# Kernel optimization log

Measured on AMD Instinct MI355X. Metric: run time of the kernel, lower is better.

The kernel has to match this reference:

```python
import jax, jax.numpy as jnp
import numpy as np

ALPHA = 0.2  # LeakyReLU negative slope
NEG_INF = -9e15


def setup_inputs() -> dict:
    key = jax.random.key(0)
    k1, k2, k3, k4 = jax.random.split(key, 4)
    B, N, Fin, Fout = 4, 4096, 128, 64
    x = jax.random.normal(k1, (B, N, Fin), dtype=jnp.float32)
    adj = jax.random.randint(k2, (B, N, N), 0, 2, dtype=jnp.int32)
    # xavier_uniform-ish init scale
    W = jax.random.normal(k3, (Fin, Fout), dtype=jnp.float32) * (1.414 / np.sqrt(Fin + Fout))
    a = jax.random.normal(k4, (3 * Fout, 1), dtype=jnp.float32) * (1.414 / np.sqrt(3 * Fout + 1))
    return {"x": x, "adj": adj, "W": W, "a": a}


def reference(x, adj, W, a):
    # h: [B, N, Fout]
    h = jnp.matmul(x, W)
    Fout = W.shape[1]
    # Original builds a_input[b,i,j] = [h_i, h_j, h_i*h_j] and dots with a.
    # Decompose a into the three blocks; identical math, no O(N^2*3F) tensor.
    a1 = a[:Fout, 0]            # weights on h_i (self)
    a2 = a[Fout:2 * Fout, 0]    # weights on h_j (neighbor)
    a3 = a[2 * Fout:, 0]        # weights on h_i * h_j (corr)
    s_self = jnp.einsum('bnf,f->bn', h, a1)        # [B,N]
    s_nei = jnp.einsum('bnf,f->bn', h, a2)         # [B,N]
    s_corr = jnp.einsum('bif,bjf->bij', h * a3, h)  # [B,N,N]
    e = s_self[:, :, None] + s_nei[:, None, :] + s_corr
    e = jnp.where(e > 0, e, ALPHA * e)  # LeakyReLU
    att = jnp.where(adj > 0, e, NEG_INF)
    att = jax.nn.softmax(att, axis=-1)
    # dropout=0.0 / eval mode -> no dropout
    h_prime = jnp.matmul(att, h)  # [B,N,Fout]
    return jax.nn.elu(h_prime)    # concat=True
```

## Files before the change

kernel.cpp:

```cpp
#include <hip/hip_runtime.h>


typedef __attribute__((ext_vector_type(4))) float f32x4;
typedef __attribute__((ext_vector_type(4))) _Float16 h16x4;
typedef __attribute__((ext_vector_type(8))) _Float16 h16x8;
typedef __attribute__((ext_vector_type(2))) __fp16 fp16x2;

#define L2E 1.4426950408889634f

__global__ __launch_bounds__(256) void gat_mask(
    const int* __restrict__ adj,
    unsigned long long* __restrict__ mask)
{
  const int tid = threadIdx.x;
  const int w = tid >> 6, lane = tid & 63;
  const size_t row = (size_t)blockIdx.x * 4 + w;
  const int* ap = adj + row * 4096 + lane;
  unsigned long long* mp = mask + row * 64;
#pragma unroll 4
  for (int s = 0; s < 64; ++s) {
    int v = ap[s * 64];
    unsigned long long m = __ballot(v > 0);
    if (lane == 0) mp[s] = m;
  }
}

__global__ __launch_bounds__(256) void gat_phase1(
    const float* __restrict__ x,
    const float* __restrict__ W,
    const float* __restrict__ a,
    _Float16* __restrict__ h16,
    _Float16* __restrict__ hT16,
    _Float16* __restrict__ q16,
    float* __restrict__ sS,
    float* __restrict__ sN)
{
  __shared__ float xs[32 * 132];
  __shared__ float ws[128 * 64];
  const int tid = threadIdx.x;
  const int bx  = blockIdx.x;
  const int b   = bx >> 7;
  const int n0  = (bx & 127) << 5;
  const float* xb = x + ((size_t)b * 4096 + n0) * 128;

#pragma unroll
  for (int p = 0; p < 4; ++p) {
    int idx = tid + p * 256;
    int row = idx >> 5, c4 = idx & 31;
    float4 v = ((const float4*)(xb + row * 128))[c4];
    *(float4*)&xs[row * 132 + c4 * 4] = v;
  }
#pragma unroll
  for (int p = 0; p < 8; ++p) {
    int idx = tid + p * 256;
    ((float4*)ws)[idx] = ((const float4*)W)[idx];
  }
  __syncthreads();

  const int tx = tid & 15;
  const int ty = tid >> 4;
  f32x4 acc0 = (f32x4){0.f, 0.f, 0.f, 0.f};
  f32x4 acc1 = (f32x4){0.f, 0.f, 0.f, 0.f};

#pragma unroll 8
  for (int k = 0; k < 128; k += 4) {
    f32x4 x0 = *(const f32x4*)&xs[(2 * ty) * 132 + k];
    f32x4 x1 = *(const f32x4*)&xs[(2 * ty + 1) * 132 + k];
    f32x4 w0 = *(const f32x4*)&ws[(k + 0) * 64 + 4 * tx];
    f32x4 w1 = *(const f32x4*)&ws[(k + 1) * 64 + 4 * tx];
    f32x4 w2 = *(const f32x4*)&ws[(k + 2) * 64 + 4 * tx];
    f32x4 w3 = *(const f32x4*)&ws[(k + 3) * 64 + 4 * tx];
    acc0 += x0.x * w0 + x0.y * w1 + x0.z * w2 + x0.w * w3;
    acc1 += x1.x * w0 + x1.y * w1 + x1.z * w2 + x1.w * w3;
  }
  float acc[2][4] = {{acc0.x, acc0.y, acc0.z, acc0.w},
                     {acc1.x, acc1.y, acc1.z, acc1.w}};

  float a1r[4], a2r[4], a3r[4];
#pragma unroll
  for (int f = 0; f < 4; ++f) {
    a1r[f] = a[4 * tx + f] * L2E;
    a2r[f] = a[64 + 4 * tx + f] * L2E;
    a3r[f] = a[128 + 4 * tx + f] * L2E;
  }
  const size_t bN = (size_t)b * 4096;
#pragma unroll
  for (int r = 0; r < 2; ++r) {
    float p1 = 0.f, p2 = 0.f;
#pragma unroll
    for (int f = 0; f < 4; ++f) { p1 += acc[r][f] * a1r[f]; p2 += acc[r][f] * a2r[f]; }
#pragma unroll
    for (int m = 1; m < 16; m <<= 1) {
      p1 += __shfl_xor(p1, m, 64);
      p2 += __shfl_xor(p2, m, 64);
    }
    if (tx == 0) {
      int n = n0 + 2 * ty + r;
      sS[bN + n] = p1;
      sN[bN + n] = p2;
    }
  }
#pragma unroll
  for (int r = 0; r < 2; ++r) {
    int n = n0 + 2 * ty + r;
    h16x4 hv, qv;
#pragma unroll
    for (int f = 0; f < 4; ++f) {
      hv[f] = (_Float16)acc[r][f];
      qv[f] = (_Float16)(acc[r][f] * a3r[f]);
    }
    *(h16x4*)&h16[(bN + n) * 64 + 4 * tx] = hv;
    *(h16x4*)&q16[(bN + n) * 64 + 4 * tx] = qv;
  }
  __syncthreads();
  _Float16* hTs = (_Float16*)xs;
#pragma unroll
  for (int f = 0; f < 4; ++f)
#pragma unroll
    for (int r = 0; r < 2; ++r)
      hTs[(4 * tx + f) * 40 + 2 * ty + r] = (_Float16)acc[r][f];
  __syncthreads();
  {
    int f = tid >> 2, part = tid & 3;
    uint4 v = *(uint4*)&hTs[f * 40 + 8 * part];
    *(uint4*)&hT16[((size_t)b * 64 + f) * 4096 + n0 + 8 * part] = v;
  }
}

__global__ __launch_bounds__(256, 4) void gat_phase2(
    const _Float16* __restrict__ h16,
    const _Float16* __restrict__ hT16,
    const _Float16* __restrict__ q16,
    const float* __restrict__ sS,
    const float* __restrict__ sN,
    const unsigned long long* __restrict__ mask,
    float* __restrict__ Opart,
    float* __restrict__ lpart)
{
  __shared__ _Float16 Kb[2][64 * 72];
  __shared__ _Float16 Tb[2][64 * 72];

  const int tid = threadIdx.x;
  const int w = tid >> 6, lane = tid & 63;
  const int qd = lane >> 4, c = lane & 15;
  const int bx = blockIdx.x;
  const int b = bx & 3;
  const int split = (bx >> 2) & 3;
  const int it = bx >> 4;
  const int i0 = it * 64 + w * 16;
  const int jq0 = split * 1024;
  const size_t bN = (size_t)b * 4096;

  const _Float16* qrow = q16 + (bN + i0 + c) * 64;
  h16x8 Qf0 = *(const h16x8*)(qrow + qd * 8);
  h16x8 Qf1 = *(const h16x8*)(qrow + 32 + qd * 8);
  const float ss = sS[bN + i0 + c];
  const int sh0 = 4 * qd;

  const unsigned long long* mrow = mask + (bN + i0 + c) * 64 + (jq0 >> 6);
  const float* snb = sN + bN + jq0 + 4 * qd;

  const int srow = tid >> 3, sc8 = (tid & 7) * 8;
  const _Float16* hsrc = h16 + (bN + jq0 + srow) * 64 + sc8;
  const _Float16* tsrc = hT16 + ((size_t)b * 64 + srow) * 4096 + jq0 + sc8;

  f32x4 O[4];
#pragma unroll
  for (int ft = 0; ft < 4; ++ft) O[ft] = (f32x4){0.f, 0.f, 0.f, 0.f};
  float lsum = 0.f;

  {
    uint4 k0 = *(const uint4*)hsrc, k1 = *(const uint4*)(hsrc + 32 * 64);
    uint4 t0 = *(const uint4*)tsrc, t1 = *(const uint4*)(tsrc + 32 * 4096);
    *(uint4*)&Kb[0][srow * 72 + sc8] = k0;
    *(uint4*)&Kb[0][(srow + 32) * 72 + sc8] = k1;
    *(uint4*)&Tb[0][srow * 72 + sc8] = t0;
    *(uint4*)&Tb[0][(srow + 32) * 72 + sc8] = t1;
  }

  for (int t = 0; t < 16; ++t) {
    const int bi = t & 1;
    unsigned long long m64 = mrow[t];
    uint4 kr0, kr1, tr0, tr1;
    if (t < 15) {
      const _Float16* hs = hsrc + (t + 1) * 64 * 64;
      const _Float16* ts = tsrc + (t + 1) * 64;
      kr0 = *(const uint4*)hs; kr1 = *(const uint4*)(hs + 32 * 64);
      tr0 = *(const uint4*)ts; tr1 = *(const uint4*)(ts + 32 * 4096);
    }
    __syncthreads();

    const _Float16* Kc = &Kb[bi][0];
    const _Float16* Tc = &Tb[bi][0];
    const int j0 = t * 64;
#pragma unroll
    for (int ct = 0; ct < 4; ++ct) {
      h16x8 Kf0 = *(const h16x8*)&Kc[(16 * ct + c) * 72 + qd * 8];
      h16x8 Kf1 = *(const h16x8*)&Kc[(16 * ct + c) * 72 + 32 + qd * 8];
      f32x4 Sv = (f32x4){0.f, 0.f, 0.f, 0.f};
      Sv = __builtin_amdgcn_mfma_f32_16x16x32_f16(Kf0, Qf0, Sv, 0, 0, 0);
      Sv = __builtin_amdgcn_mfma_f32_16x16x32_f16(Kf1, Qf1, Sv, 0, 0, 0);

      f32x4 snv = *(const f32x4*)(snb + j0 + 16 * ct);
      f32x4 ev = Sv + snv + ss;
      f32x4 tv = __builtin_elementwise_max(ev, ev * 0.2f);
      unsigned int bits = (unsigned int)(m64 >> (sh0 + 16 * ct));
      float p0 = __builtin_amdgcn_exp2f(tv.x);
      float p1 = __builtin_amdgcn_exp2f(tv.y);
      float p2 = __builtin_amdgcn_exp2f(tv.z);
      float p3 = __builtin_amdgcn_exp2f(tv.w);
      p0 = (bits & 1u) ? p0 : 0.f;
      p1 = (bits & 2u) ? p1 : 0.f;
      p2 = (bits & 4u) ? p2 : 0.f;
      p3 = (bits & 8u) ? p3 : 0.f;
      lsum += (p0 + p1) + (p2 + p3);
      fp16x2 plo = __builtin_amdgcn_cvt_pkrtz(p0, p1);
      fp16x2 phi = __builtin_amdgcn_cvt_pkrtz(p2, p3);
      h16x4 Pf = (h16x4){(_Float16)plo.x, (_Float16)plo.y,
                         (_Float16)phi.x, (_Float16)phi.y};

#pragma unroll
      for (int ft = 0; ft < 4; ++ft) {
        h16x4 Vf = *(const h16x4*)&Tc[(16 * ft + c) * 72 + 16 * ct + 4 * qd];
        O[ft] = __builtin_amdgcn_mfma_f32_16x16x16f16(Vf, Pf, O[ft], 0, 0, 0);
      }
    }

    if (t < 15) {
      *(uint4*)&Kb[bi ^ 1][srow * 72 + sc8] = kr0;
      *(uint4*)&Kb[bi ^ 1][(srow + 32) * 72 + sc8] = kr1;
      *(uint4*)&Tb[bi ^ 1][srow * 72 + sc8] = tr0;
      *(uint4*)&Tb[bi ^ 1][(srow + 32) * 72 + sc8] = tr1;
    }
  }

  lsum += __shfl_xor(lsum, 16, 64);
  lsum += __shfl_xor(lsum, 32, 64);

  float* orow = Opart + ((size_t)split * 16384 + bN + i0 + c) * 64;
#pragma unroll
  for (int ft = 0; ft < 4; ++ft)
    *(f32x4*)(orow + 16 * ft + 4 * qd) = O[ft];
  if (lane < 16) lpart[split * 16384 + bN + i0 + c] = lsum;
}

__global__ __launch_bounds__(256) void gat_combine(
    const float* __restrict__ Opart, const float* __restrict__ lpart,
    float* __restrict__ out)
{
  const int tid = threadIdx.x;
  const size_t row = (size_t)blockIdx.x * 16 + (tid >> 4);
  const int f4 = (tid & 15) * 4;
  const size_t R = 16384;
  float l = lpart[row] + lpart[R + row] + lpart[2 * R + row] + lpart[3 * R + row];
  f32x4 o = *(const f32x4*)&Opart[row * 64 + f4];
  o += *(const f32x4*)&Opart[(R + row) * 64 + f4];
  o += *(const f32x4*)&Opart[(2 * R + row) * 64 + f4];
  o += *(const f32x4*)&Opart[(3 * R + row) * 64 + f4];
  float inv = 1.0f / l;
  float4 res;
  float v;
  v = o.x * inv; res.x = v > 0.f ? v : __expf(v) - 1.f;
  v = o.y * inv; res.y = v > 0.f ? v : __expf(v) - 1.f;
  v = o.z * inv; res.z = v > 0.f ? v : __expf(v) - 1.f;
  v = o.w * inv; res.w = v > 0.f ? v : __expf(v) - 1.f;
  *(float4*)&out[row * 64 + f4] = res;
}

extern "C" void kernel_launch(void* const* d_in, const int* in_sizes, int n_in,
                              void* d_out, int out_size, void* d_ws, size_t ws_size,
                              hipStream_t stream) {
  const float* x  = (const float*)d_in[0];
  const int* adj  = (const int*)d_in[1];
  const float* W  = (const float*)d_in[2];
  const float* a  = (const float*)d_in[3];
  float* out = (float*)d_out;

  char* ws = (char*)d_ws;
  _Float16* h16  = (_Float16*)(ws);
  _Float16* hT16 = (_Float16*)(ws + (2u << 20));
  _Float16* q16  = (_Float16*)(ws + (4u << 20));
  float* sS = (float*)(ws + (6u << 20));
  float* sN = (float*)(ws + (6u << 20) + (64u << 10));
  float* Opart = (float*)(ws + (6u << 20) + (128u << 10));
  float* lpart = (float*)(ws + (6u << 20) + (128u << 10) + (16u << 20));
  unsigned long long* mask =
      (unsigned long long*)(ws + (6u << 20) + (128u << 10) + (16u << 20) + (256u << 10));

  gat_mask<<<4096, 256, 0, stream>>>(adj, mask);
  gat_phase1<<<512, 256, 0, stream>>>(x, W, a, h16, hT16, q16, sS, sN);
  gat_phase2<<<1024, 256, 0, stream>>>(h16, hT16, q16, sS, sN, mask, Opart, lpart);
  gat_combine<<<1024, 256, 0, stream>>>(Opart, lpart, out);
}
```

Measured before the change: 448.3 us.

## Process two query row tiles per wave with swizzled LDS and 8-way key split

Each wave in phase 2 now handles 32 query rows (two 16-row tiles) and reuses every loaded K and V fragment for both. This halves LDS reads per MFMA. The key dimension is split 8 ways instead of 4, so the grid keeps 1024 blocks. The padded LDS layout is replaced with an XOR swizzle to avoid bank conflicts, and sN is staged in LDS. The cost is more registers, twice as many partial outputs written, and a combine step that reduces 8 partials instead of 4.

```diff
diff --git a/kernel.cpp b/kernel.cpp
--- a/kernel.cpp
+++ b/kernel.cpp
@@ -137,111 +137,162 @@
     float* __restrict__ Opart,
     float* __restrict__ lpart)
 {
-  __shared__ _Float16 Kb[2][64 * 72];
-  __shared__ _Float16 Tb[2][64 * 72];
+  __shared__ _Float16 Kb[2][4096];
+  __shared__ _Float16 Tb[2][4096];
+  __shared__ float sNl[512];
 
   const int tid = threadIdx.x;
   const int w = tid >> 6, lane = tid & 63;
   const int qd = lane >> 4, c = lane & 15;
   const int bx = blockIdx.x;
   const int b = bx & 3;
-  const int split = (bx >> 2) & 3;
-  const int it = bx >> 4;
-  const int i0 = it * 64 + w * 16;
-  const int jq0 = split * 1024;
+  const int split = (bx >> 2) & 7;
+  const int it = bx >> 5;
+  const int i0 = it * 128 + w * 32;
+  const int jq0 = split * 512;
   const size_t bN = (size_t)b * 4096;
 
-  const _Float16* qrow = q16 + (bN + i0 + c) * 64;
-  h16x8 Qf0 = *(const h16x8*)(qrow + qd * 8);
-  h16x8 Qf1 = *(const h16x8*)(qrow + 32 + qd * 8);
-  const float ss = sS[bN + i0 + c];
-  const int sh0 = 4 * qd;
-
-  const unsigned long long* mrow = mask + (bN + i0 + c) * 64 + (jq0 >> 6);
-  const float* snb = sN + bN + jq0 + 4 * qd;
-
-  const int srow = tid >> 3, sc8 = (tid & 7) * 8;
-  const _Float16* hsrc = h16 + (bN + jq0 + srow) * 64 + sc8;
-  const _Float16* tsrc = hT16 + ((size_t)b * 64 + srow) * 4096 + jq0 + sc8;
-
-  f32x4 O[4];
-#pragma unroll
-  for (int ft = 0; ft < 4; ++ft) O[ft] = (f32x4){0.f, 0.f, 0.f, 0.f};
-  float lsum = 0.f;
+  const _Float16* qA = q16 + (bN + i0 + c) * 64;
+  const _Float16* qB = q16 + (bN + i0 + 16 + c) * 64;
+  h16x8 QA0 = *(const h16x8*)(qA + qd * 8);
+  h16x8 QA1 = *(const h16x8*)(qA + 32 + qd * 8);
+  h16x8 QB0 = *(const h16x8*)(qB + qd * 8);
+  h16x8 QB1 = *(const h16x8*)(qB + 32 + qd * 8);
+  const float ssA = sS[bN + i0 + c];
+  const float ssB = sS[bN + i0 + 16 + c];
+
+  const unsigned long long* mpA = mask + (bN + i0 + c) * 64 + (jq0 >> 6);
+  const unsigned long long* mpB = mask + (bN + i0 + 16 + c) * 64 + (jq0 >> 6);
+
+  const int srow = tid >> 3, chunk = tid & 7;
+  const int ksw = (chunk ^ (srow & 7)) << 3;
+  const int tsw = (chunk ^ ((srow >> 1) & 7)) << 3;
+  const bool tswap = (srow & 1);
+  const _Float16* hsrc = h16 + (bN + jq0 + srow) * 64 + chunk * 8;
+  const _Float16* tsrc = hT16 + ((size_t)b * 64 + srow) * 4096 + jq0 + chunk * 8;
+
+  f32x4 OA[4], OB[4];
+#pragma unroll
+  for (int ft = 0; ft < 4; ++ft) {
+    OA[ft] = (f32x4){0.f, 0.f, 0.f, 0.f};
+    OB[ft] = (f32x4){0.f, 0.f, 0.f, 0.f};
+  }
+  float lsumA = 0.f, lsumB = 0.f;
 
   {
     uint4 k0 = *(const uint4*)hsrc, k1 = *(const uint4*)(hsrc + 32 * 64);
     uint4 t0 = *(const uint4*)tsrc, t1 = *(const uint4*)(tsrc + 32 * 4096);
-    *(uint4*)&Kb[0][srow * 72 + sc8] = k0;
-    *(uint4*)&Kb[0][(srow + 32) * 72 + sc8] = k1;
-    *(uint4*)&Tb[0][srow * 72 + sc8] = t0;
-    *(uint4*)&Tb[0][(srow + 32) * 72 + sc8] = t1;
-  }
-
-  for (int t = 0; t < 16; ++t) {
-    const int bi = t & 1;
-    unsigned long long m64 = mrow[t];
+    *(uint4*)&Kb[0][srow * 64 + ksw] = k0;
+    *(uint4*)&Kb[0][(srow + 32) * 64 + ksw] = k1;
+    uint4 s0 = tswap ? (uint4){t0.z, t0.w, t0.x, t0.y} : t0;
+    uint4 s1 = tswap ? (uint4){t1.z, t1.w, t1.x, t1.y} : t1;
+    *(uint4*)&Tb[0][srow * 64 + tsw] = s0;
+    *(uint4*)&Tb[0][(srow + 32) * 64 + tsw] = s1;
+  }
+  if (tid < 128) ((f32x4*)sNl)[tid] = *(const f32x4*)(sN + bN + jq0 + tid * 4);
+  unsigned long long mA = mpA[0], mB = mpB[0];
+
+  for (int t = 0; t < 8; ++t) {
+    __syncthreads();
+
     uint4 kr0, kr1, tr0, tr1;
-    if (t < 15) {
-      const _Float16* hs = hsrc + (t + 1) * 64 * 64;
+    unsigned long long mAn = mA, mBn = mB;
+    if (t < 7) {
+      const _Float16* hs = hsrc + (t + 1) * 4096;
       const _Float16* ts = tsrc + (t + 1) * 64;
       kr0 = *(const uint4*)hs; kr1 = *(const uint4*)(hs + 32 * 64);
       tr0 = *(const uint4*)ts; tr1 = *(const uint4*)(ts + 32 * 4096);
-    }
-    __syncthreads();
-
-    const _Float16* Kc = &Kb[bi][0];
-    const _Float16* Tc = &Tb[bi][0];
-    const int j0 = t * 64;
+      mAn = mpA[t + 1]; mBn = mpB[t + 1];
+    }
+
+    const _Float16* Kc = &Kb[t & 1][0];
+    const _Float16* Tc = &Tb[t & 1][0];
 #pragma unroll
     for (int ct = 0; ct < 4; ++ct) {
-      h16x8 Kf0 = *(const h16x8*)&Kc[(16 * ct + c) * 72 + qd * 8];
-      h16x8 Kf1 = *(const h16x8*)&Kc[(16 * ct + c) * 72 + 32 + qd * 8];
-      f32x4 Sv = (f32x4){0.f, 0.f, 0.f, 0.f};
-      Sv = __builtin_amdgcn_mfma_f32_16x16x32_f16(Kf0, Qf0, Sv, 0, 0, 0);
-      Sv = __builtin_amdgcn_mfma_f32_16x16x32_f16(Kf1, Qf1, Sv, 0, 0, 0);
-
-      f32x4 snv = *(const f32x4*)(snb + j0 + 16 * ct);
-      f32x4 ev = Sv + snv + ss;
-      f32x4 tv = __builtin_elementwise_max(ev, ev * 0.2f);
-      unsigned int bits = (unsigned int)(m64 >> (sh0 + 16 * ct));
-      float p0 = __builtin_amdgcn_exp2f(tv.x);
-      float p1 = __builtin_amdgcn_exp2f(tv.y);
-      float p2 = __builtin_amdgcn_exp2f(tv.z);
-      float p3 = __builtin_amdgcn_exp2f(tv.w);
-      p0 = (bits & 1u) ? p0 : 0.f;
-      p1 = (bits & 2u) ? p1 : 0.f;
-      p2 = (bits & 4u) ? p2 : 0.f;
-      p3 = (bits & 8u) ? p3 : 0.f;
-      lsum += (p0 + p1) + (p2 + p3);
-      fp16x2 plo = __builtin_amdgcn_cvt_pkrtz(p0, p1);
-      fp16x2 phi = __builtin_amdgcn_cvt_pkrtz(p2, p3);
-      h16x4 Pf = (h16x4){(_Float16)plo.x, (_Float16)plo.y,
-                         (_Float16)phi.x, (_Float16)phi.y};
+      const int krow = 16 * ct + c;
+      h16x8 Kf0 = *(const h16x8*)&Kc[krow * 64 + ((qd ^ (c & 7)) << 3)];
+      h16x8 Kf1 = *(const h16x8*)&Kc[krow * 64 + (((qd + 4) ^ (c & 7)) << 3)];
+      f32x4 SvA = (f32x4){0.f, 0.f, 0.f, 0.f};
+      SvA = __builtin_amdgcn_mfma_f32_16x16x32_f16(Kf0, QA0, SvA, 0, 0, 0);
+      SvA = __builtin_amdgcn_mfma_f32_16x16x32_f16(Kf1, QA1, SvA, 0, 0, 0);
+      f32x4 SvB = (f32x4){0.f, 0.f, 0.f, 0.f};
+      SvB = __builtin_amdgcn_mfma_f32_16x16x32_f16(Kf0, QB0, SvB, 0, 0, 0);
+      SvB = __builtin_amdgcn_mfma_f32_16x16x32_f16(Kf1, QB1, SvB, 0, 0, 0);
+
+      f32x4 snv = ((const f32x4*)sNl)[t * 16 + 4 * ct + qd];
+      const int sh = 16 * ct + 4 * qd;
+
+      f32x4 evA = SvA + snv + ssA;
+      f32x4 tvA = __builtin_elementwise_max(evA, evA * 0.2f);
+      unsigned bA = (unsigned)(mA >> sh);
+      float a0 = __builtin_amdgcn_exp2f(tvA.x);
+      float a1 = __builtin_amdgcn_exp2f(tvA.y);
+      float a2 = __builtin_amdgcn_exp2f(tvA.z);
+      float a3 = __builtin_amdgcn_exp2f(tvA.w);
+      a0 = (bA & 1u) ? a0 : 0.f;
+      a1 = (bA & 2u) ? a1 : 0.f;
+      a2 = (bA & 4u) ? a2 : 0.f;
+      a3 = (bA & 8u) ? a3 : 0.f;
+      lsumA += (a0 + a1) + (a2 + a3);
+      fp16x2 al = __builtin_amdgcn_cvt_pkrtz(a0, a1);
+      fp16x2 ah = __builtin_amdgcn_cvt_pkrtz(a2, a3);
+      h16x4 PfA = (h16x4){(_Float16)al.x, (_Float16)al.y,
+                          (_Float16)ah.x, (_Float16)ah.y};
+
+      f32x4 evB = SvB + snv + ssB;
+      f32x4 tvB = __builtin_elementwise_max(evB, evB * 0.2f);
+      unsigned bB = (unsigned)(mB >> sh);
+      float b0 = __builtin_amdgcn_exp2f(tvB.x);
+      float b1 = __builtin_amdgcn_exp2f(tvB.y);
+      float b2 = __builtin_amdgcn_exp2f(tvB.z);
+      float b3 = __builtin_amdgcn_exp2f(tvB.w);
+      b0 = (bB & 1u) ? b0 : 0.f;
+      b1 = (bB & 2u) ? b1 : 0.f;
+      b2 = (bB & 4u) ? b2 : 0.f;
+      b3 = (bB & 8u) ? b3 : 0.f;
+      lsumB += (b0 + b1) + (b2 + b3);
+      fp16x2 bl = __builtin_amdgcn_cvt_pkrtz(b0, b1);
+      fp16x2 bh = __builtin_amdgcn_cvt_pkrtz(b2, b3);
+      h16x4 PfB = (h16x4){(_Float16)bl.x, (_Float16)bl.y,
+                          (_Float16)bh.x, (_Float16)bh.y};
 
 #pragma unroll
       for (int ft = 0; ft < 4; ++ft) {
-        h16x4 Vf = *(const h16x4*)&Tc[(16 * ft + c) * 72 + 16 * ct + 4 * qd];
-        O[ft] = __builtin_amdgcn_mfma_f32_16x16x16f16(Vf, Pf, O[ft], 0, 0, 0);
+        h16x4 Vf = *(const h16x4*)&Tc[(16 * ft + c) * 64 +
+                                      (((4 * ct + qd) ^ c) << 2)];
+        OA[ft] = __builtin_amdgcn_mfma_f32_16x16x16f16(Vf, PfA, OA[ft], 0, 0, 0);
+        OB[ft] = __builtin_amdgcn_mfma_f32_16x16x16f16(Vf, PfB, OB[ft], 0, 0, 0);
       }
     }
 
-    if (t < 15) {
-      *(uint4*)&Kb[bi ^ 1][srow * 72 + sc8] = kr0;
-      *(uint4*)&Kb[bi ^ 1][(srow + 32) * 72 + sc8] = kr1;
-      *(uint4*)&Tb[bi ^ 1][srow * 72 + sc8] = tr0;
-      *(uint4*)&Tb[bi ^ 1][(srow + 32) * 72 + sc8] = tr1;
-    }
-  }
-
-  lsum += __shfl_xor(lsum, 16, 64);
-  lsum += __shfl_xor(lsum, 32, 64);
-
-  float* orow = Opart + ((size_t)split * 16384 + bN + i0 + c) * 64;
-#pragma unroll
-  for (int ft = 0; ft < 4; ++ft)
-    *(f32x4*)(orow + 16 * ft + 4 * qd) = O[ft];
-  if (lane < 16) lpart[split * 16384 + bN + i0 + c] = lsum;
+    if (t < 7) {
+      _Float16* K2 = &Kb[(t & 1) ^ 1][0];
+      _Float16* T2 = &Tb[(t & 1) ^ 1][0];
+      *(uint4*)&K2[srow * 64 + ksw] = kr0;
+      *(uint4*)&K2[(srow + 32) * 64 + ksw] = kr1;
+      uint4 s0 = tswap ? (uint4){tr0.z, tr0.w, tr0.x, tr0.y} : tr0;
+      uint4 s1 = tswap ? (uint4){tr1.z, tr1.w, tr1.x, tr1.y} : tr1;
+      *(uint4*)&T2[srow * 64 + tsw] = s0;
+      *(uint4*)&T2[(srow + 32) * 64 + tsw] = s1;
+    }
+    mA = mAn; mB = mBn;
+  }
+
+  lsumA += __shfl_xor(lsumA, 16, 64);
+  lsumA += __shfl_xor(lsumA, 32, 64);
+  lsumB += __shfl_xor(lsumB, 16, 64);
+  lsumB += __shfl_xor(lsumB, 32, 64);
+
+  const size_t sbase = (size_t)split * 16384 + bN;
+  float* orowA = Opart + (sbase + i0 + c) * 64;
+  float* orowB = Opart + (sbase + i0 + 16 + c) * 64;
+#pragma unroll
+  for (int ft = 0; ft < 4; ++ft) {
+    *(f32x4*)(orowA + 16 * ft + 4 * qd) = OA[ft];
+    *(f32x4*)(orowB + 16 * ft + 4 * qd) = OB[ft];
+  }
+  if (qd == 0) lpart[sbase + i0 + c] = lsumA;
+  if (qd == 1) lpart[sbase + i0 + 16 + c] = lsumB;
 }
 
 __global__ __launch_bounds__(256) void gat_combine(
@@ -252,11 +303,13 @@
   const size_t row = (size_t)blockIdx.x * 16 + (tid >> 4);
   const int f4 = (tid & 15) * 4;
   const size_t R = 16384;
-  float l = lpart[row] + lpart[R + row] + lpart[2 * R + row] + lpart[3 * R + row];
-  f32x4 o = *(const f32x4*)&Opart[row * 64 + f4];
-  o += *(const f32x4*)&Opart[(R + row) * 64 + f4];
-  o += *(const f32x4*)&Opart[(2 * R + row) * 64 + f4];
-  o += *(const f32x4*)&Opart[(3 * R + row) * 64 + f4];
+  float l = 0.f;
+  f32x4 o = (f32x4){0.f, 0.f, 0.f, 0.f};
+#pragma unroll
+  for (int s = 0; s < 8; ++s) {
+    l += lpart[s * R + row];
+    o += *(const f32x4*)&Opart[(s * R + row) * 64 + f4];
+  }
   float inv = 1.0f / l;
   float4 res;
   float v;
@@ -283,9 +336,9 @@
   float* sS = (float*)(ws + (6u << 20));
   float* sN = (float*)(ws + (6u << 20) + (64u << 10));
   float* Opart = (float*)(ws + (6u << 20) + (128u << 10));
-  float* lpart = (float*)(ws + (6u << 20) + (128u << 10) + (16u << 20));
+  float* lpart = (float*)(ws + (6u << 20) + (128u << 10) + (34u << 20));
   unsigned long long* mask =
-      (unsigned long long*)(ws + (6u << 20) + (128u << 10) + (16u << 20) + (256u << 10));
+      (unsigned long long*)(ws + (6u << 20) + (128u << 10) + (35u << 20));
 
   gat_mask<<<4096, 256, 0, stream>>>(adj, mask);
   gat_phase1<<<512, 256, 0, stream>>>(x, W, a, h16, hT16, q16, sS, sN);
```

New measurement: 478.6 us. +6.8%, slower.
